# Performance work log

Hardware: AMD Instinct MI355X
Metric: run time of the kernel (lower is better)

Reference implementation:

```python
import jax, jax.numpy as jnp
import numpy as np

N_LAYERS = 2  # args.n_layers


def expmap0(u):
    """Hyperboloid (K=1/c, c=1) exponential map at the origin.
    u: [N, d] Euclidean tangent vector (spatial part; time coord is 0).
    Returns [N, d+1] point on the hyperboloid: (cosh||u||, sinh||u||*u/||u||).
    This matches Hyperboloid.expmap0(proj_tan0(cat([zeros, u], -1))) with c=1.
    """
    theta = jnp.sqrt(jnp.sum(u * u, axis=-1, keepdims=True))
    theta = jnp.maximum(theta, 1e-7)
    x0 = jnp.cosh(theta)
    xs = jnp.sinh(theta) * (u / theta)
    return jnp.concatenate([x0, xs], axis=-1)


def setup_inputs() -> dict:
    key = jax.random.key(0)
    k1, k2, k3, k4 = jax.random.split(key, 4)
    n_users, n_items, d, E = 100000, 150000, 64, 4000000
    N = n_users + n_items
    return {
        "user_emb": jax.random.normal(k1, (n_users, d), jnp.float32) * 0.1,
        "item_emb": jax.random.normal(k2, (n_items, d), jnp.float32) * 0.1,
        "h_list": jax.random.randint(k3, (E,), 0, N, dtype=jnp.int32),
        "t_list": jax.random.randint(k4, (E,), 0, N, dtype=jnp.int32),
    }


def reference(user_emb, item_emb, h_list, t_list):
    N = user_emb.shape[0] + item_emb.shape[0]
    dtype = user_emb.dtype

    # _cal_sparse_adj: symmetric normalization G = D^-1/2 A D^-1/2 in COO form
    deg = jax.ops.segment_sum(jnp.ones_like(h_list, dtype), h_list, num_segments=N)
    deg = jnp.maximum(deg, 1.0)
    g_values = jax.lax.rsqrt(deg[h_list] * deg[t_list])  # [E]

    # LightGCN-style propagation: x_{l+1} = G @ x_l, layer sum / mean
    x = jnp.concatenate([user_emb, item_emb], axis=0)  # [N, d]
    out = x
    for _ in range(N_LAYERS):
        msg = g_values[:, None] * x[t_list]              # [E, d] gather
        x = jax.ops.segment_sum(msg, h_list, num_segments=N)  # scatter-add SpMM
        out = out + x
    out = out / (N_LAYERS + 1)

    # Hyperbolic lift of the aggregated embeddings (zerou/zeroi + expmap0, c=1)
    h = expmap0(out)  # [N, d+1]

    return jnp.concatenate([out, h], axis=-1)  # [N, 2d+1]
```

## Files before the change

### kernel.cpp

```cpp
#include <hip/hip_runtime.h>

#define DIM 64
#define CHUNK 16384
#define BSHIFT 11
#define BSIZE (1 << BSHIFT)
#define MAXB 128
#define TBITS 21
#define TMASK ((1u << TBITS) - 1u)

__device__ __forceinline__ unsigned f2bf(float f) {
    unsigned u = __float_as_uint(f);
    return (u + 0x7FFFu + ((u >> 16) & 1u)) >> 16;
}
__device__ __forceinline__ float bflo(unsigned u) {
    return __uint_as_float(u << 16);
}
__device__ __forceinline__ float bfhi(unsigned u) {
    return __uint_as_float(u & 0xFFFF0000u);
}

__global__ void zero_u32(unsigned* __restrict__ p, int n) {
    int i = blockIdx.x * blockDim.x + threadIdx.x;
    int stride = gridDim.x * blockDim.x;
    for (; i < n; i += stride) p[i] = 0u;
}

__global__ void bucket_hist(const int* __restrict__ h, unsigned* __restrict__ bcount,
                            int E, int nb) {
    __shared__ unsigned s[MAXB];
    for (int i = threadIdx.x; i < nb; i += blockDim.x) s[i] = 0u;
    __syncthreads();
    int i = blockIdx.x * blockDim.x + threadIdx.x;
    int stride = gridDim.x * blockDim.x;
    for (; i < E; i += stride) atomicAdd(&s[((unsigned)h[i]) >> BSHIFT], 1u);
    __syncthreads();
    for (int i = threadIdx.x; i < nb; i += blockDim.x)
        if (s[i]) atomicAdd(&bcount[i], s[i]);
}

__global__ void bucket_scan(const unsigned* __restrict__ bcount,
                            unsigned* __restrict__ bbase, unsigned* __restrict__ bcur,
                            unsigned* __restrict__ row_ptr, int nb, int N, int E) {
    __shared__ unsigned s[MAXB];
    int tid = threadIdx.x;
    unsigned v = (tid < nb) ? bcount[tid] : 0u;
    s[tid] = v; __syncthreads();
    for (int off = 1; off < MAXB; off <<= 1) {
        unsigned t = (tid >= off) ? s[tid - off] : 0u;
        __syncthreads();
        s[tid] += t; __syncthreads();
    }
    if (tid < nb) {
        unsigned ex = s[tid] - v;
        bbase[tid] = ex;
        bcur[tid] = ex;
    }
    if (tid == 0) {
        bbase[nb] = (unsigned)E;
        row_ptr[N] = (unsigned)E;
    }
}

__global__ void partition_edges(const int* __restrict__ h, const int* __restrict__ t,
                                unsigned* __restrict__ bcur, unsigned* __restrict__ tmp,
                                int E, int nb) {
    __shared__ unsigned cnt[MAXB];
    int tid = threadIdx.x;
    long start = (long)blockIdx.x * CHUNK;
    long end = start + CHUNK; if (end > E) end = E;
    for (int i = tid; i < nb; i += blockDim.x) cnt[i] = 0u;
    __syncthreads();
    for (long i = start + tid; i < end; i += blockDim.x)
        atomicAdd(&cnt[((unsigned)h[i]) >> BSHIFT], 1u);
    __syncthreads();
    for (int i = tid; i < nb; i += blockDim.x) {
        unsigned c = cnt[i];
        cnt[i] = c ? atomicAdd(&bcur[i], c) : 0u;
    }
    __syncthreads();
    for (long i = start + tid; i < end; i += blockDim.x) {
        unsigned hn = (unsigned)h[i], tn = (unsigned)t[i];
        unsigned pos = atomicAdd(&cnt[hn >> BSHIFT], 1u);
        tmp[pos] = ((hn & (BSIZE - 1)) << TBITS) | tn;
    }
}

__global__ void build_csr_bucket(const unsigned* __restrict__ tmp,
                                 const unsigned* __restrict__ bbase,
                                 unsigned* __restrict__ row_ptr,
                                 float* __restrict__ rdeg,
                                 float* __restrict__ rsq,
                                 int* __restrict__ col, int N) {
    __shared__ unsigned cnt[BSIZE];
    __shared__ unsigned cur[BSIZE];
    __shared__ unsigned ts[512];
    int b = blockIdx.x;
    int tid = threadIdx.x;
    unsigned e0 = bbase[b], e1 = bbase[b + 1];
    int nlo = b << BSHIFT;
    int nloc = N - nlo; if (nloc > BSIZE) nloc = BSIZE;
    for (int i = tid; i < nloc; i += 512) cnt[i] = 0u;
    __syncthreads();
    for (unsigned i = e0 + tid; i < e1; i += 512)
        atomicAdd(&cnt[tmp[i] >> TBITS], 1u);
    __syncthreads();
    int base = tid * 4;
    unsigned mysum = 0;
    #pragma unroll
    for (int j = 0; j < 4; ++j) { int i = base + j; if (i < nloc) mysum += cnt[i]; }
    ts[tid] = mysum; __syncthreads();
    for (int off = 1; off < 512; off <<= 1) {
        unsigned t = (tid >= off) ? ts[tid - off] : 0u;
        __syncthreads();
        ts[tid] += t; __syncthreads();
    }
    unsigned off0 = ts[tid] - mysum;
    #pragma unroll
    for (int j = 0; j < 4; ++j) {
        int i = base + j;
        if (i < nloc) {
            unsigned c = cnt[i];
            float d = fmaxf((float)c, 1.0f);
            cur[i] = off0;
            row_ptr[nlo + i] = e0 + off0;
            rdeg[nlo + i] = rsqrtf(d);
            rsq[nlo + i]  = sqrtf(d);
            off0 += c;
        }
    }
    __syncthreads();
    for (unsigned i = e0 + tid; i < e1; i += 512) {
        unsigned pk = tmp[i];
        unsigned pos = e0 + atomicAdd(&cur[pk >> TBITS], 1u);
        col[pos] = (int)(pk & TMASK);
    }
}

__global__ void cvt_x0s(const float* __restrict__ ue, const float* __restrict__ ie,
                        long nu_elems, const float* __restrict__ rdeg,
                        unsigned short* __restrict__ x0s, long M) {
    long i4 = ((long)blockIdx.x * blockDim.x + threadIdx.x) * 4;
    long stride = (long)gridDim.x * blockDim.x * 4;
    for (; i4 < M; i4 += stride) {
        const float* src = (i4 < nu_elems) ? ue + i4 : ie + (i4 - nu_elems);
        float rd = rdeg[i4 >> 6];
        float4 v = *(const float4*)src;
        ushort4 o;
        o.x = (unsigned short)f2bf(rd * v.x); o.y = (unsigned short)f2bf(rd * v.y);
        o.z = (unsigned short)f2bf(rd * v.z); o.w = (unsigned short)f2bf(rd * v.w);
        *(ushort4*)(x0s + i4) = o;
    }
}

__global__ void spmm_pull_l1(const unsigned* __restrict__ rp,
                             const int* __restrict__ col,
                             const float* __restrict__ rdeg,
                             const uint4* __restrict__ x0s,
                             uint4* __restrict__ x1s, int N) {
    int node = blockIdx.x * (blockDim.x >> 3) + (threadIdx.x >> 3);
    int l = threadIdx.x & 7;
    if (node >= N) return;
    int e0 = (int)rp[node], e1 = (int)rp[node + 1];
    float a0 = 0.f, a1 = 0.f, a2 = 0.f, a3 = 0.f;
    float a4 = 0.f, a5 = 0.f, a6 = 0.f, a7 = 0.f;
    int e = e0;
    for (; e + 4 <= e1; e += 4) {
        int c0 = col[e], c1 = col[e + 1], c2 = col[e + 2], c3 = col[e + 3];
        uint4 u0 = x0s[((size_t)c0 << 3) + l];
        uint4 u1 = x0s[((size_t)c1 << 3) + l];
        uint4 u2 = x0s[((size_t)c2 << 3) + l];
        uint4 u3 = x0s[((size_t)c3 << 3) + l];
        a0 += bflo(u0.x) + bflo(u1.x) + bflo(u2.x) + bflo(u3.x);
        a1 += bfhi(u0.x) + bfhi(u1.x) + bfhi(u2.x) + bfhi(u3.x);
        a2 += bflo(u0.y) + bflo(u1.y) + bflo(u2.y) + bflo(u3.y);
        a3 += bfhi(u0.y) + bfhi(u1.y) + bfhi(u2.y) + bfhi(u3.y);
        a4 += bflo(u0.z) + bflo(u1.z) + bflo(u2.z) + bflo(u3.z);
        a5 += bfhi(u0.z) + bfhi(u1.z) + bfhi(u2.z) + bfhi(u3.z);
        a6 += bflo(u0.w) + bflo(u1.w) + bflo(u2.w) + bflo(u3.w);
        a7 += bfhi(u0.w) + bfhi(u1.w) + bfhi(u2.w) + bfhi(u3.w);
    }
    for (; e < e1; ++e) {
        int c = col[e];
        uint4 u = x0s[((size_t)c << 3) + l];
        a0 += bflo(u.x); a1 += bfhi(u.x);
        a2 += bflo(u.y); a3 += bfhi(u.y);
        a4 += bflo(u.z); a5 += bfhi(u.z);
        a6 += bflo(u.w); a7 += bfhi(u.w);
    }
    float rd = rdeg[node];
    float rd2 = rd * rd;
    uint4 o;
    o.x = (f2bf(rd2 * a1) << 16) | f2bf(rd2 * a0);
    o.y = (f2bf(rd2 * a3) << 16) | f2bf(rd2 * a2);
    o.z = (f2bf(rd2 * a5) << 16) | f2bf(rd2 * a4);
    o.w = (f2bf(rd2 * a7) << 16) | f2bf(rd2 * a6);
    x1s[((size_t)node << 3) + l] = o;
}

__global__ void spmm_l2_finalize(const unsigned* __restrict__ rp,
                                 const int* __restrict__ col,
                                 const float* __restrict__ rdeg,
                                 const float* __restrict__ rsq,
                                 const uint4* __restrict__ x0s,
                                 const uint4* __restrict__ x1s,
                                 float* __restrict__ out, int N) {
    int node = blockIdx.x * (blockDim.x >> 3) + (threadIdx.x >> 3);
    int l = threadIdx.x & 7;
    if (node >= N) return;
    int e0 = (int)rp[node], e1 = (int)rp[node + 1];
    float a0 = 0.f, a1 = 0.f, a2 = 0.f, a3 = 0.f;
    float a4 = 0.f, a5 = 0.f, a6 = 0.f, a7 = 0.f;
    int e = e0;
    for (; e + 4 <= e1; e += 4) {
        int c0 = col[e], c1 = col[e + 1], c2 = col[e + 2], c3 = col[e + 3];
        uint4 u0 = x1s[((size_t)c0 << 3) + l];
        uint4 u1 = x1s[((size_t)c1 << 3) + l];
        uint4 u2 = x1s[((size_t)c2 << 3) + l];
        uint4 u3 = x1s[((size_t)c3 << 3) + l];
        a0 += bflo(u0.x) + bflo(u1.x) + bflo(u2.x) + bflo(u3.x);
        a1 += bfhi(u0.x) + bfhi(u1.x) + bfhi(u2.x) + bfhi(u3.x);
        a2 += bflo(u0.y) + bflo(u1.y) + bflo(u2.y) + bflo(u3.y);
        a3 += bfhi(u0.y) + bfhi(u1.y) + bfhi(u2.y) + bfhi(u3.y);
        a4 += bflo(u0.z) + bflo(u1.z) + bflo(u2.z) + bflo(u3.z);
        a5 += bfhi(u0.z) + bfhi(u1.z) + bfhi(u2.z) + bfhi(u3.z);
        a6 += bflo(u0.w) + bflo(u1.w) + bflo(u2.w) + bflo(u3.w);
        a7 += bfhi(u0.w) + bfhi(u1.w) + bfhi(u2.w) + bfhi(u3.w);
    }
    for (; e < e1; ++e) {
        int c = col[e];
        uint4 u = x1s[((size_t)c << 3) + l];
        a0 += bflo(u.x); a1 += bfhi(u.x);
        a2 += bflo(u.y); a3 += bfhi(u.y);
        a4 += bflo(u.z); a5 += bfhi(u.z);
        a6 += bflo(u.w); a7 += bfhi(u.w);
    }
    float rd = rdeg[node];
    a0 *= rd; a1 *= rd; a2 *= rd; a3 *= rd;
    a4 *= rd; a5 *= rd; a6 *= rd; a7 *= rd;
    float rq = rsq[node];
    uint4 u0 = x0s[((size_t)node << 3) + l];
    uint4 u1 = x1s[((size_t)node << 3) + l];
    float v0 = (rq * (bflo(u0.x) + bflo(u1.x)) + a0) * (1.0f / 3.0f);
    float v1 = (rq * (bfhi(u0.x) + bfhi(u1.x)) + a1) * (1.0f / 3.0f);
    float v2 = (rq * (bflo(u0.y) + bflo(u1.y)) + a2) * (1.0f / 3.0f);
    float v3 = (rq * (bfhi(u0.y) + bfhi(u1.y)) + a3) * (1.0f / 3.0f);
    float v4 = (rq * (bflo(u0.z) + bflo(u1.z)) + a4) * (1.0f / 3.0f);
    float v5 = (rq * (bfhi(u0.z) + bfhi(u1.z)) + a5) * (1.0f / 3.0f);
    float v6 = (rq * (bflo(u0.w) + bflo(u1.w)) + a6) * (1.0f / 3.0f);
    float v7 = (rq * (bfhi(u0.w) + bfhi(u1.w)) + a7) * (1.0f / 3.0f);
    float ss = v0*v0 + v1*v1 + v2*v2 + v3*v3 + v4*v4 + v5*v5 + v6*v6 + v7*v7;
    ss += __shfl_xor(ss, 1);
    ss += __shfl_xor(ss, 2);
    ss += __shfl_xor(ss, 4);
    float theta = fmaxf(sqrtf(ss), 1e-7f);
    float ex  = __expf(theta);
    float exi = __builtin_amdgcn_rcpf(ex);
    float sh = 0.5f * (ex - exi);
    float ch = 0.5f * (ex + exi);
    float sc = sh * __builtin_amdgcn_rcpf(theta);
    float* o = out + (long)node * 129;
    *(float4*)(o + 8 * l)     = make_float4(v0, v1, v2, v3);
    *(float4*)(o + 8 * l + 4) = make_float4(v4, v5, v6, v7);
    if (l == 0) o[64] = ch;
    *(float4*)(o + 65 + 8 * l)     = make_float4(sc*v0, sc*v1, sc*v2, sc*v3);
    *(float4*)(o + 65 + 8 * l + 4) = make_float4(sc*v4, sc*v5, sc*v6, sc*v7);
}

extern "C" void kernel_launch(void* const* d_in, const int* in_sizes, int n_in,
                              void* d_out, int out_size, void* d_ws, size_t ws_size,
                              hipStream_t stream) {
    const float* ue = (const float*)d_in[0];
    const float* ie = (const float*)d_in[1];
    const int*   hl = (const int*)d_in[2];
    const int*   tl = (const int*)d_in[3];
    float* out = (float*)d_out;

    const int n_users = in_sizes[0] / DIM;
    const int n_items = in_sizes[1] / DIM;
    const int N = n_users + n_items;
    const int E = in_sizes[2];
    const int nb = (N + BSIZE - 1) >> BSHIFT;
    const long M = (long)N * DIM;

    auto align = [](size_t x) { return (x + 255) & ~(size_t)255; };
    char* p = (char*)d_ws;
    unsigned* row_ptr = (unsigned*)p;            p += align((size_t)(N + 1) * 4);
    float*    rdeg    = (float*)p;               p += align((size_t)N * 4);
    float*    rsq     = (float*)p;               p += align((size_t)N * 4);
    unsigned* bcount  = (unsigned*)p;            p += align((size_t)MAXB * 4);
    unsigned* bbase   = (unsigned*)p;            p += align((size_t)(MAXB + 1) * 4);
    unsigned* bcur    = (unsigned*)p;            p += align((size_t)MAXB * 4);
    int*      col     = (int*)p;                 p += align((size_t)E * 4);
    unsigned* tmp     = (unsigned*)p;            p += align((size_t)E * 4);
    unsigned short* x0sh = (unsigned short*)p;   p += align((size_t)M * 2);
    unsigned short* x1sh = (unsigned short*)p;
    const uint4* x0s = (const uint4*)x0sh;
    uint4* x1s = (uint4*)x1sh;

    zero_u32<<<1, 256, 0, stream>>>(bcount, MAXB);

    bucket_hist<<<512, 256, 0, stream>>>(hl, bcount, E, nb);

    bucket_scan<<<1, MAXB, 0, stream>>>(bcount, bbase, bcur, row_ptr, nb, N, E);

    {
        int blocks = (E + CHUNK - 1) / CHUNK;
        partition_edges<<<blocks, 256, 0, stream>>>(hl, tl, bcur, tmp, E, nb);
    }

    build_csr_bucket<<<nb, 512, 0, stream>>>(tmp, bbase, row_ptr, rdeg, rsq, col, N);

    {
        long threads = (M + 3) / 4;
        int blocks = (int)((threads + 255) / 256);
        cvt_x0s<<<blocks, 256, 0, stream>>>(ue, ie, (long)n_users * DIM, rdeg, x0sh, M);
    }

    {
        int nodes_per_block = 256 / 8;
        int blocks = (N + nodes_per_block - 1) / nodes_per_block;
        spmm_pull_l1<<<blocks, 256, 0, stream>>>(row_ptr, col, rdeg, x0s, x1s, N);
    }

    {
        int nodes_per_block = 256 / 8;
        int blocks = (N + nodes_per_block - 1) / nodes_per_block;
        spmm_l2_finalize<<<blocks, 256, 0, stream>>>(row_ptr, col, rdeg, rsq,
                                                     x0s, x1s, out, N);
    }
}
```

Baseline: 338.2 us.

## Fuse bf16 scaled x0 conversion into CSR bucket build and halve bucket size

Removes the separate cvt_x0s kernel and performs the degree-scaled bf16 conversion of the input embeddings inside build_csr_bucket, reusing the per-node degree counts already in shared memory. Bucket size is halved (BSHIFT 11→10, MAXB 128→256), so there are twice as many CSR-build blocks, each covering 1024 nodes with 2 nodes per thread in the scan. This saves one launch and a reread of rdeg, and gives more parallelism in the bucket build. The risk is fewer edges per block, which means more partition atomics and more bucket overhead; with 250k nodes the number of buckets stays under 256.

Measured after the change: 333.2 us. No clear change (-1.5%).

```diff
diff --git a/kernel.cpp b/kernel.cpp
--- a/kernel.cpp
+++ b/kernel.cpp
@@ -2,9 +2,9 @@
 
 #define DIM 64
 #define CHUNK 16384
-#define BSHIFT 11
+#define BSHIFT 10
 #define BSIZE (1 << BSHIFT)
-#define MAXB 128
+#define MAXB 256
 #define TBITS 21
 #define TMASK ((1u << TBITS) - 1u)
 
@@ -90,7 +90,11 @@
                                  unsigned* __restrict__ row_ptr,
                                  float* __restrict__ rdeg,
                                  float* __restrict__ rsq,
-                                 int* __restrict__ col, int N) {
+                                 int* __restrict__ col,
+                                 const float* __restrict__ ue,
+                                 const float* __restrict__ ie,
+                                 int n_users,
+                                 unsigned short* __restrict__ x0s, int N) {
     __shared__ unsigned cnt[BSIZE];
     __shared__ unsigned cur[BSIZE];
     __shared__ unsigned ts[512];
@@ -104,10 +108,10 @@
     for (unsigned i = e0 + tid; i < e1; i += 512)
         atomicAdd(&cnt[tmp[i] >> TBITS], 1u);
     __syncthreads();
-    int base = tid * 4;
+    int base = tid * 2;
     unsigned mysum = 0;
     #pragma unroll
-    for (int j = 0; j < 4; ++j) { int i = base + j; if (i < nloc) mysum += cnt[i]; }
+    for (int j = 0; j < 2; ++j) { int i = base + j; if (i < nloc) mysum += cnt[i]; }
     ts[tid] = mysum; __syncthreads();
     for (int off = 1; off < 512; off <<= 1) {
         unsigned t = (tid >= off) ? ts[tid - off] : 0u;
@@ -116,7 +120,7 @@
     }
     unsigned off0 = ts[tid] - mysum;
     #pragma unroll
-    for (int j = 0; j < 4; ++j) {
+    for (int j = 0; j < 2; ++j) {
         int i = base + j;
         if (i < nloc) {
             unsigned c = cnt[i];
@@ -134,21 +138,19 @@
         unsigned pos = e0 + atomicAdd(&cur[pk >> TBITS], 1u);
         col[pos] = (int)(pk & TMASK);
     }
-}
-
-__global__ void cvt_x0s(const float* __restrict__ ue, const float* __restrict__ ie,
-                        long nu_elems, const float* __restrict__ rdeg,
-                        unsigned short* __restrict__ x0s, long M) {
-    long i4 = ((long)blockIdx.x * blockDim.x + threadIdx.x) * 4;
-    long stride = (long)gridDim.x * blockDim.x * 4;
-    for (; i4 < M; i4 += stride) {
-        const float* src = (i4 < nu_elems) ? ue + i4 : ie + (i4 - nu_elems);
-        float rd = rdeg[i4 >> 6];
+    long nu_elems = (long)n_users * DIM;
+    int total = nloc * 16;
+    for (int idx = tid; idx < total; idx += 512) {
+        int i = idx >> 4, j = idx & 15;
+        long n = (long)(nlo + i);
+        long elem = n * DIM + j * 4;
+        const float* src = (elem < nu_elems) ? ue + elem : ie + (elem - nu_elems);
+        float rd = rsqrtf(fmaxf((float)cnt[i], 1.0f));
         float4 v = *(const float4*)src;
         ushort4 o;
         o.x = (unsigned short)f2bf(rd * v.x); o.y = (unsigned short)f2bf(rd * v.y);
         o.z = (unsigned short)f2bf(rd * v.z); o.w = (unsigned short)f2bf(rd * v.w);
-        *(ushort4*)(x0s + i4) = o;
+        *(ushort4*)(x0s + elem) = o;
     }
 }
 
@@ -308,13 +310,8 @@
         partition_edges<<<blocks, 256, 0, stream>>>(hl, tl, bcur, tmp, E, nb);
     }
 
-    build_csr_bucket<<<nb, 512, 0, stream>>>(tmp, bbase, row_ptr, rdeg, rsq, col, N);
-
-    {
-        long threads = (M + 3) / 4;
-        int blocks = (int)((threads + 255) / 256);
-        cvt_x0s<<<blocks, 256, 0, stream>>>(ue, ie, (long)n_users * DIM, rdeg, x0sh, M);
-    }
+    build_csr_bucket<<<nb, 512, 0, stream>>>(tmp, bbase, row_ptr, rdeg, rsq, col,
+                                             ue, ie, n_users, x0sh, N);
 
     {
         int nodes_per_block = 256 / 8;
```
